# Optimization experiments

Measured on AMD Instinct MI355X. Metric: run time of the kernel, lower is better.

The kernel has to match this reference:

```python
import jax, jax.numpy as jnp
import numpy as np

N_BINS = 15  # matches __init__ default


def setup_inputs() -> dict:
    key = jax.random.key(0)
    k1, k2 = jax.random.split(key)
    N, C = 100000, 1000
    softmaxes_probs = jax.random.uniform(k1, (N, C), dtype=jnp.float32)
    labels = jax.random.randint(k2, (N,), 0, C, dtype=jnp.int64)
    return {"softmaxes_probs": softmaxes_probs, "labels": labels}


def reference(softmaxes_probs, labels):
    # Classwise ECE: for each class c and bin b = (b/n_bins, (b+1)/n_bins],
    #   sce_c = sum_b |avg_conf_in_bin - acc_in_bin| * (count_in_bin / N)
    # returned value is mean_c sce_c.
    n_bins = N_BINS
    N, C = softmaxes_probs.shape
    conf = softmaxes_probs  # [N, C]

    # bin index: conf in (b/n_bins, (b+1)/n_bins] -> b ; conf <= 0 -> -1 (no bin)
    bin_idx = jnp.ceil(conf * n_bins).astype(jnp.int32) - 1
    bin_idx = jnp.minimum(bin_idx, n_bins - 1)
    valid = bin_idx >= 0

    class_ids = jnp.arange(C, dtype=jnp.int32)[None, :]  # [1, C]
    # combined segment id per (sample, class); invalid entries go to a dump segment
    seg = jnp.where(valid, bin_idx + class_ids * n_bins, C * n_bins)  # [N, C]
    seg_flat = seg.ravel()
    num_seg = C * n_bins + 1

    ones = jnp.ones_like(conf)
    counts = jax.ops.segment_sum(ones.ravel(), seg_flat, num_segments=num_seg)[:-1].reshape(C, n_bins)
    conf_sum = jax.ops.segment_sum(conf.ravel(), seg_flat, num_segments=num_seg)[:-1].reshape(C, n_bins)
    # labels_in_class broadcast to [N, C]
    correct = (labels[:, None] == jnp.arange(C, dtype=labels.dtype)[None, :]).astype(conf.dtype)
    correct_sum = jax.ops.segment_sum(correct.ravel(), seg_flat, num_segments=num_seg)[:-1].reshape(C, n_bins)

    prop_in_bin = counts / N  # prop_in_bin = in_bin.float().mean() over N samples
    nonempty = counts > 0
    denom = jnp.maximum(counts, 1.0)
    acc_in_bin = correct_sum / denom
    avg_conf_in_bin = conf_sum / denom
    contrib = jnp.where(nonempty, jnp.abs(avg_conf_in_bin - acc_in_bin) * prop_in_bin, 0.0)
    per_class_sce = jnp.sum(contrib, axis=1)  # [C]
    return jnp.mean(per_class_sce)
```

## Files before the change

kernel.cpp:

```cpp
#include <hip/hip_runtime.h>


#define NBINS   15
#define THREADS 512
#define PSTRIDE 17
#define LDSW    (THREADS * PSTRIDE)
#define CORW    3840
#define SLABH   (THREADS * NBINS)
#define RBLK    120
#define Q40     1099511627776.0f

__global__ __launch_bounds__(THREADS, 6) void ece_hist(
    const float* __restrict__ probs, const int* __restrict__ labels,
    int N, int C, int R,
    unsigned* __restrict__ partial,
    unsigned long long* __restrict__ accum,
    unsigned* __restrict__ doneCnt)
{
    __shared__ unsigned sA[LDSW];
    __shared__ unsigned sCorW[CORW];
    const int t = threadIdx.x;
    if (blockIdx.x == 0 && t == 0) { *accum = 0ull; *doneCnt = 0u; }
    #pragma unroll
    for (int i = t; i < LDSW; i += THREADS) sA[i] = 0u;
    #pragma unroll
    for (int i = t; i < CORW; i += THREADS) sCorW[i] = 0u;
    __syncthreads();

    const int cls0 = 2 * t;
    const bool live = (cls0 + 1 < C);
    const int col  = live ? cls0 : 0;

    const int r0 = blockIdx.x * R;
    int rend = N - r0; if (rend > R) rend = R; if (rend < 0) rend = 0;

    const float2* p = (const float2*)(probs + (size_t)r0 * C + col);
    const size_t rowstep = (size_t)(C >> 1);
    unsigned* s0 = sA + t * PSTRIDE;

    float2 bufA[8], bufB[8];
    int    labA[8], labB[8];

    #define LOADG(buf, lab, base)                                          \
        _Pragma("unroll")                                                  \
        for (int k = 0; k < 8; ++k) {                                      \
            int ri = (base) + k;                                           \
            ri = ri < rend ? ri : rend - 1;                                \
            buf[k] = live ? p[(size_t)ri * rowstep] : make_float2(0.f,0.f);\
            lab[k] = labels[r0 + ri];                                      \
        }

    #define PROC1(v, lb)                                                   \
        {                                                                  \
            int b0 = (int)(v.x * 15.0f);   \
            b0 = b0 < NBINS - 1 ? b0 : NBINS - 1;                          \
            unsigned c0 = (unsigned)fmaf(v.x, 128.0f, 0.5f);               \
            atomicAdd(&s0[b0], (v.x > 0.0f) ? c0 : 0u);                    \
            int b1 = (int)(v.y * 15.0f);                                   \
            b1 = b1 < NBINS - 1 ? b1 : NBINS - 1;                          \
            unsigned c1 = (unsigned)fmaf(v.y, 128.0f, 0.5f);               \
            atomicAdd(&s0[b1], (v.y > 0.0f) ? (c1 << 16) : 0u);            \
            if ((lb) == cls0 && v.x > 0.0f) {                              \
                int sl = (lb) * NBINS + b0;                                \
                atomicAdd(&sCorW[sl >> 2], 1u << (8 * (sl & 3)));          \
            } else if ((lb) == cls0 + 1 && v.y > 0.0f) {                   \
                int sl = (lb) * NBINS + b1;                                \
                atomicAdd(&sCorW[sl >> 2], 1u << (8 * (sl & 3)));          \
            }                                                              \
        }

    #define PROCG(buf, lab)                                                \
        _Pragma("unroll")                                                  \
        for (int k = 0; k < 8; ++k) PROC1(buf[k], lab[k])

    int r = 0;
    if (rend >= 16) {
        LOADG(bufA, labA, 0);
        for (; r + 16 <= rend; r += 16) {
            LOADG(bufB, labB, r + 8);
            PROCG(bufA, labA);
            LOADG(bufA, labA, r + 16);
            PROCG(bufB, labB);
        }
    }
    for (; r < rend; ++r) {
        float2 v = live ? p[(size_t)r * rowstep] : make_float2(0.f, 0.f);
        int lb = labels[r0 + r];
        PROC1(v, lb);
    }
    __syncthreads();

    const unsigned char* sCorB = (const unsigned char*)sCorW;
    unsigned* dst = partial + (size_t)blockIdx.x * SLABH;
    #pragma unroll
    for (int i = t; i < SLABH; i += THREADS) {
        int o = i / NBINS, j = i - o * NBINS;
        unsigned w = sA[o * PSTRIDE + j];
        int s0c = (int)(w & 0xFFFFu) - 128 * (int)sCorB[(2 * o) * NBINS + j];
        int s1c = (int)(w >> 16)     - 128 * (int)sCorB[(2 * o + 1) * NBINS + j];
        dst[i] = ((unsigned)s0c & 0xFFFFu) | ((unsigned)s1c << 16);
    }
}

__global__ __launch_bounds__(1024, 1) void ece_red(
    const unsigned* __restrict__ partial, int chunks, int C, int N,
    unsigned long long* __restrict__ accum, unsigned* __restrict__ doneCnt,
    float* __restrict__ out)
{
    __shared__ int sq0[16][64];
    __shared__ int sq1[16][64];
    const int t = threadIdx.x;
    const int g = t >> 6, pj = t & 63;
    const int pair = blockIdx.x * 64 + pj;

    const int gsz = (chunks + 15) >> 4;
    int k0 = g * gsz;
    int k1 = k0 + gsz; if (k1 > chunks) k1 = chunks;
    int a0 = 0, a1 = 0;
    #pragma unroll 8
    for (int k = k0; k < k1; ++k) {
        unsigned w = partial[(size_t)k * SLABH + pair];
        a0 += (int)(short)(w & 0xFFFFu);
        a1 += (int)(short)(w >> 16);
    }
    sq0[g][pj] = a0;
    sq1[g][pj] = a1;
    __syncthreads();

    if (t < 64) {
        int t0 = 0, t1 = 0;
        #pragma unroll
        for (int gg = 0; gg < 16; ++gg) { t0 += sq0[gg][t]; t1 += sq1[gg][t]; }
        int pr = blockIdx.x * 64 + t;
        int o  = pr / NBINS;
        float contrib = 0.0f;
        if (2 * o     < C) contrib += fabsf((float)t0);
        if (2 * o + 1 < C) contrib += fabsf((float)t1);
        contrib *= (1.0f / 128.0f) * (1.0f / (float)N);
        for (int off = 32; off; off >>= 1) contrib += __shfl_down(contrib, off);
        if (t == 0) {
            atomicAdd(accum, (unsigned long long)(contrib * Q40));
            __threadfence();
            if (atomicAdd(doneCnt, 1u) == (unsigned)(RBLK - 1)) {
                __threadfence();
                unsigned long long a = atomicAdd(accum, 0ull);
                out[0] = (float)((double)a * (1.0 / (double)Q40) / (double)C);
            }
        }
    }
}

extern "C" void kernel_launch(void* const* d_in, const int* in_sizes, int n_in,
                              void* d_out, int out_size, void* d_ws, size_t ws_size,
                              hipStream_t stream) {
    const float* probs  = (const float*)d_in[0];
    const int*   labels = (const int*)d_in[1];
    const int N = in_sizes[1];
    const int C = in_sizes[0] / N;

    const size_t headBytes = 4096;
    const size_t slabBytes = (size_t)SLABH * 4;

    unsigned long long* accum   = (unsigned long long*)d_ws;
    unsigned*           doneCnt = (unsigned*)((char*)d_ws + 8);
    unsigned*           partial = (unsigned*)((char*)d_ws + headBytes);

    long long avail = (long long)ws_size - (long long)headBytes;
    int chunks = (int)(avail / (long long)slabBytes);
    if (chunks > 512) chunks = 512;
    if (chunks < 393) chunks = 393;
    const int R = (N + chunks - 1) / chunks;

    ece_hist<<<chunks, THREADS, 0, stream>>>(probs, labels, N, C, R,
                                             partial, accum, doneCnt);
    ece_red<<<RBLK, 1024, 0, stream>>>(partial, chunks, C, N,
                                       accum, doneCnt, (float*)d_out);
}
```

Baseline: 94.33 us.

## Use one class per thread and fold correctness into the histogram atomic

The histogram kernel now runs 1024 threads per block, one class per thread with scalar loads, instead of 512 threads handling a float2 class pair. Each thread's single LDS atomic adds the scaled confidence minus 128 when the label matches, so the separate byte-packed correct-count array and its conditional atomics go away. Pairs are packed into 16-bit halves only at the final write-out. Global loads become nontemporal. The costs are narrower 4-byte loads per thread, more threads contending for LDS, and 32-bit per-class LDS words whose low 16 bits must not overflow per block.

```diff
diff --git a/kernel.cpp b/kernel.cpp
--- a/kernel.cpp
+++ b/kernel.cpp
@@ -2,15 +2,14 @@
 
 
 #define NBINS   15
-#define THREADS 512
+#define THREADS 1024
 #define PSTRIDE 17
 #define LDSW    (THREADS * PSTRIDE)
-#define CORW    3840
-#define SLABH   (THREADS * NBINS)
+#define SLABH   7680
 #define RBLK    120
 #define Q40     1099511627776.0f
 
-__global__ __launch_bounds__(THREADS, 6) void ece_hist(
+__global__ __launch_bounds__(THREADS, 8) void ece_hist(
     const float* __restrict__ probs, const int* __restrict__ labels,
     int N, int C, int R,
     unsigned* __restrict__ partial,
@@ -18,59 +17,46 @@
     unsigned* __restrict__ doneCnt)
 {
     __shared__ unsigned sA[LDSW];
-    __shared__ unsigned sCorW[CORW];
     const int t = threadIdx.x;
     if (blockIdx.x == 0 && t == 0) { *accum = 0ull; *doneCnt = 0u; }
     #pragma unroll
     for (int i = t; i < LDSW; i += THREADS) sA[i] = 0u;
-    #pragma unroll
-    for (int i = t; i < CORW; i += THREADS) sCorW[i] = 0u;
     __syncthreads();
 
-    const int cls0 = 2 * t;
-    const bool live = (cls0 + 1 < C);
-    const int col  = live ? cls0 : 0;
+    const int cls  = t;
+    const bool live = (cls < C);
+    const int col  = live ? cls : 0;
 
     const int r0 = blockIdx.x * R;
     int rend = N - r0; if (rend > R) rend = R; if (rend < 0) rend = 0;
 
-    const float2* p = (const float2*)(probs + (size_t)r0 * C + col);
-    const size_t rowstep = (size_t)(C >> 1);
+    const float* p = probs + (size_t)r0 * C + col;
     unsigned* s0 = sA + t * PSTRIDE;
 
-    float2 bufA[8], bufB[8];
-    int    labA[8], labB[8];
+    float bufA[8], bufB[8];
+    int   labA[8], labB[8];
 
-    #define LOADG(buf, lab, base)                                          \
-        _Pragma("unroll")                                                  \
-        for (int k = 0; k < 8; ++k) {                                      \
-            int ri = (base) + k;                                           \
-            ri = ri < rend ? ri : rend - 1;                                \
-            buf[k] = live ? p[(size_t)ri * rowstep] : make_float2(0.f,0.f);\
-            lab[k] = labels[r0 + ri];                                      \
+    #define LOADG(buf, lab, base)                                           \
+        _Pragma("unroll")                                                   \
+        for (int k = 0; k < 8; ++k) {                                       \
+            int ri = (base) + k;                                            \
+            ri = ri < rend ? ri : rend - 1;                                 \
+            buf[k] = live ? __builtin_nontemporal_load(&p[(size_t)ri * C])  \
+                          : 0.0f;                                           \
+            lab[k] = labels[r0 + ri];                                       \
         }
 
-    #define PROC1(v, lb)                                                   \
-        {                                                                  \
-            int b0 = (int)(v.x * 15.0f);   \
-            b0 = b0 < NBINS - 1 ? b0 : NBINS - 1;                          \
-            unsigned c0 = (unsigned)fmaf(v.x, 128.0f, 0.5f);               \
-            atomicAdd(&s0[b0], (v.x > 0.0f) ? c0 : 0u);                    \
-            int b1 = (int)(v.y * 15.0f);                                   \
-            b1 = b1 < NBINS - 1 ? b1 : NBINS - 1;                          \
-            unsigned c1 = (unsigned)fmaf(v.y, 128.0f, 0.5f);               \
-            atomicAdd(&s0[b1], (v.y > 0.0f) ? (c1 << 16) : 0u);            \
-            if ((lb) == cls0 && v.x > 0.0f) {                              \
-                int sl = (lb) * NBINS + b0;                                \
-                atomicAdd(&sCorW[sl >> 2], 1u << (8 * (sl & 3)));          \
-            } else if ((lb) == cls0 + 1 && v.y > 0.0f) {                   \
-                int sl = (lb) * NBINS + b1;                                \
-                atomicAdd(&sCorW[sl >> 2], 1u << (8 * (sl & 3)));          \
-            }                                                              \
+    #define PROC1(v, lb)                                                    \
+        {                                                                   \
+            int b = (int)((v) * 15.0f);     \
+            b = b < NBINS - 1 ? b : NBINS - 1;                              \
+            unsigned c = (unsigned)fmaf((v), 128.0f, 0.5f);                 \
+            c += ((lb) == cls) ? (unsigned)(-128) : 0u;  \
+            atomicAdd(&s0[b], ((v) > 0.0f) ? c : 0u);    \
         }
 
-    #define PROCG(buf, lab)                                                \
-        _Pragma("unroll")                                                  \
+    #define PROCG(buf, lab)                                                 \
+        _Pragma("unroll")                                                   \
         for (int k = 0; k < 8; ++k) PROC1(buf[k], lab[k])
 
     int r = 0;
@@ -84,21 +70,19 @@
         }
     }
     for (; r < rend; ++r) {
-        float2 v = live ? p[(size_t)r * rowstep] : make_float2(0.f, 0.f);
+        float v = live ? p[(size_t)r * C] : 0.0f;
         int lb = labels[r0 + r];
         PROC1(v, lb);
     }
     __syncthreads();
 
-    const unsigned char* sCorB = (const unsigned char*)sCorW;
     unsigned* dst = partial + (size_t)blockIdx.x * SLABH;
     #pragma unroll
     for (int i = t; i < SLABH; i += THREADS) {
         int o = i / NBINS, j = i - o * NBINS;
-        unsigned w = sA[o * PSTRIDE + j];
-        int s0c = (int)(w & 0xFFFFu) - 128 * (int)sCorB[(2 * o) * NBINS + j];
-        int s1c = (int)(w >> 16)     - 128 * (int)sCorB[(2 * o + 1) * NBINS + j];
-        dst[i] = ((unsigned)s0c & 0xFFFFu) | ((unsigned)s1c << 16);
+        unsigned v0 = sA[(2 * o) * PSTRIDE + j];
+        unsigned v1 = sA[(2 * o + 1) * PSTRIDE + j];
+        dst[i] = (v0 & 0xFFFFu) | (v1 << 16);
     }
 }
 
```

Result: faster. 91.69 us (-2.8%).
